# Kernel optimization log

Measured on AMD Instinct MI355X. Metric: run time of the kernel, lower is better.

The kernel has to match this reference:

```python
import jax, jax.numpy as jnp
import numpy as np

VOCAB = 267735
CUTOFFS = [0, 20000, 40000, 200000, 267735]
D_EMBED = 1024
D_PROJ = 1024
DIV_VAL = 4
EMB_SCALE = float(D_PROJ) ** 0.5


def setup_inputs() -> dict:
    key = jax.random.key(0)
    ks = jax.random.split(key, 9)
    input_ids = jax.random.randint(ks[0], (8, 2048), 0, VOCAB, dtype=jnp.int64)
    inp = {"input_ids": input_ids}
    for i in range(4):
        l, r = CUTOFFS[i], CUTOFFS[i + 1]
        d_i = D_EMBED // (DIV_VAL ** i)
        inp[f"emb{i}"] = jax.random.normal(ks[1 + 2 * i], (r - l, d_i), dtype=jnp.float32) * 0.02
        inp[f"proj{i}"] = jax.random.normal(ks[2 + 2 * i], (D_PROJ, d_i), dtype=jnp.float32) * 0.02
    return inp


def reference(input_ids, emb0, emb1, emb2, emb3, proj0, proj1, proj2, proj3):
    tables = [emb0, emb1, emb2, emb3]
    projs = [proj0, proj1, proj2, proj3]
    out = jnp.zeros(input_ids.shape + (D_PROJ,), dtype=jnp.float32)
    for i in range(4):
        l, r = CUTOFFS[i], CUTOFFS[i + 1]
        mask = (input_ids >= l) & (input_ids < r)                     # [B,S]
        idx = jnp.clip(input_ids - l, 0, r - l - 1)                   # [B,S]
        emb_i = tables[i][idx]                                        # [B,S,d_i]
        proj_i = jnp.einsum('bse,de->bsd', emb_i, projs[i])           # [B,S,D]
        out = out + jnp.where(mask[..., None], proj_i, 0.0)
    return out * EMB_SCALE
```

## Files before the change

### kernel.cpp

```cpp
#include <hip/hip_runtime.h>


constexpr int NTOK  = 16384;
constexpr int DPROJ = 1024;
constexpr float EMB_SCALE = 32.0f;

typedef __attribute__((ext_vector_type(8))) short short8;
typedef __attribute__((ext_vector_type(4))) float float4v;

__global__ __launch_bounds__(256) void partition_kernel(
    const int* __restrict__ ids, int* __restrict__ cnt, int* __restrict__ lists)
{
    int t = blockIdx.x * 256 + threadIdx.x;
    int id = ids[t];
    int c = (id >= 200000) ? 3 : (id >= 40000) ? 2 : (id >= 20000) ? 1 : 0;
    int lane = threadIdx.x & 63;
    unsigned long long lt = (1ull << lane) - 1ull;
    int pos = 0;
#pragma unroll
    for (int i = 0; i < 4; ++i) {
        unsigned long long m = __ballot(c == i);
        int b = 0;
        if (lane == 0 && m) b = atomicAdd(&cnt[i], (int)__popcll(m));
        b = __shfl(b, 0);
        if (c == i) pos = b + (int)__popcll(m & lt);
    }
    lists[c * NTOK + pos] = t;
}

__device__ __forceinline__ short f2bf(float f) {
    unsigned u = __builtin_bit_cast(unsigned, f);
    u += 0x7FFFu + ((u >> 16) & 1u);
    return (short)(u >> 16);
}

template<int D>
__device__ __forceinline__ void gemm_tile(
    const int* __restrict__ ids,
    const float* __restrict__ emb,
    const float* __restrict__ proj,
    const int* __restrict__ list,
    int count, int lo,
    float* __restrict__ out,
    short (*Asm)[40], short (*Bsm)[40], int* smTok, int* smRow)
{
    const int m0 = blockIdx.y * 64;
    if (m0 >= count) return;
    const int n0 = blockIdx.x * 128;
    const int tid  = threadIdx.x;
    const int lane = tid & 63;
    const int wv   = tid >> 6;
    const int col  = lane & 15;
    const int quad = lane >> 4;

    if (tid < 64) {
        int m = m0 + tid;
        int tok = (m < count) ? list[m] : -1;
        smTok[tid] = tok;
        smRow[tid] = (tok >= 0) ? (ids[tok] - lo) : 0;
    }
    __syncthreads();

    const int ar = tid >> 2, ac = (tid & 3) * 8;
    const int br = tid >> 1, bc = (tid & 1) * 16;
    const float* arow = emb  + (size_t)smRow[ar] * D + ac;
    const float* brow = proj + (size_t)(n0 + br) * D + bc;

    float4v acc[4][2] = {};

    constexpr int CHUNKS = (D + 31) / 32;
    for (int kc = 0; kc < CHUNKS; ++kc) {
        const int k0 = kc * 32;
        float4 a0 = {}, a1 = {}, b0 = {}, b1 = {}, b2 = {}, b3 = {};
        if (ac + 0  < D || D >= 32) {  }
        if (D >= 32 || ac + 0  < D) a0 = *(const float4*)(arow + k0);
        if (D >= 32 || ac + 4  < D) a1 = *(const float4*)(arow + k0 + 4);
        if (D >= 32 || bc + 0  < D) b0 = *(const float4*)(brow + k0);
        if (D >= 32 || bc + 4  < D) b1 = *(const float4*)(brow + k0 + 4);
        if (D >= 32 || bc + 8  < D) b2 = *(const float4*)(brow + k0 + 8);
        if (D >= 32 || bc + 12 < D) b3 = *(const float4*)(brow + k0 + 12);
        if (D == 16) {
            if (ac >= 16) { a0 = float4{}; a1 = float4{}; }
            if (bc >= 16) { b0 = float4{}; b1 = float4{}; b2 = float4{}; b3 = float4{}; }
        }
        __syncthreads();
        {
            short8 va = { f2bf(a0.x), f2bf(a0.y), f2bf(a0.z), f2bf(a0.w),
                          f2bf(a1.x), f2bf(a1.y), f2bf(a1.z), f2bf(a1.w) };
            *(short8*)&Asm[ar][ac] = va;
            short8 vb0 = { f2bf(b0.x), f2bf(b0.y), f2bf(b0.z), f2bf(b0.w),
                           f2bf(b1.x), f2bf(b1.y), f2bf(b1.z), f2bf(b1.w) };
            short8 vb1 = { f2bf(b2.x), f2bf(b2.y), f2bf(b2.z), f2bf(b2.w),
                           f2bf(b3.x), f2bf(b3.y), f2bf(b3.z), f2bf(b3.w) };
            *(short8*)&Bsm[br][bc]     = vb0;
            *(short8*)&Bsm[br][bc + 8] = vb1;
        }
        __syncthreads();

        short8 af[4], bf[2];
#pragma unroll
        for (int m = 0; m < 4; ++m)
            af[m] = *(const short8*)&Asm[m * 16 + col][quad * 8];
#pragma unroll
        for (int n = 0; n < 2; ++n)
            bf[n] = *(const short8*)&Bsm[wv * 32 + n * 16 + col][quad * 8];
#pragma unroll
        for (int m = 0; m < 4; ++m)
#pragma unroll
            for (int n = 0; n < 2; ++n)
                acc[m][n] = __builtin_amdgcn_mfma_f32_16x16x32_bf16(
                    af[m], bf[n], acc[m][n], 0, 0, 0);
    }

#pragma unroll
    for (int m = 0; m < 4; ++m) {
#pragma unroll
        for (int r = 0; r < 4; ++r) {
            int tok = smTok[m * 16 + quad * 4 + r];
            if (tok < 0) continue;
            float* op = out + (size_t)tok * DPROJ + n0 + wv * 32 + col;
            op[0]  = acc[m][0][r] * EMB_SCALE;
            op[16] = acc[m][1][r] * EMB_SCALE;
        }
    }
}

__global__ __launch_bounds__(256) void adaptive_emb_gemm(
    const int* __restrict__ ids,
    const float* __restrict__ e0, const float* __restrict__ p0,
    const float* __restrict__ e1, const float* __restrict__ p1,
    const float* __restrict__ e2, const float* __restrict__ p2,
    const float* __restrict__ e3, const float* __restrict__ p3,
    const int* __restrict__ cnt, const int* __restrict__ lists,
    float* __restrict__ out)
{
    __shared__ short Asm[64][40];
    __shared__ short Bsm[128][40];
    __shared__ int smTok[64];
    __shared__ int smRow[64];

    switch (blockIdx.z) {
    case 0: gemm_tile<1024>(ids, e0, p0, lists,          cnt[0], 0,      out, Asm, Bsm, smTok, smRow); break;
    case 1: gemm_tile<256> (ids, e1, p1, lists + NTOK,   cnt[1], 20000,  out, Asm, Bsm, smTok, smRow); break;
    case 2: gemm_tile<64>  (ids, e2, p2, lists + 2*NTOK, cnt[2], 40000,  out, Asm, Bsm, smTok, smRow); break;
    case 3: gemm_tile<16>  (ids, e3, p3, lists + 3*NTOK, cnt[3], 200000, out, Asm, Bsm, smTok, smRow); break;
    }
}

extern "C" void kernel_launch(void* const* d_in, const int* in_sizes, int n_in,
                              void* d_out, int out_size, void* d_ws, size_t ws_size,
                              hipStream_t stream) {
    const int*   ids = (const int*)d_in[0];
    const float* e0  = (const float*)d_in[1];
    const float* p0  = (const float*)d_in[2];
    const float* e1  = (const float*)d_in[3];
    const float* p1  = (const float*)d_in[4];
    const float* e2  = (const float*)d_in[5];
    const float* p2  = (const float*)d_in[6];
    const float* e3  = (const float*)d_in[7];
    const float* p3  = (const float*)d_in[8];
    float* out = (float*)d_out;

    int* cnt   = (int*)d_ws;
    int* lists = cnt + 4;

    hipMemsetAsync(cnt, 0, 4 * sizeof(int), stream);
    partition_kernel<<<dim3(NTOK / 256), 256, 0, stream>>>(ids, cnt, lists);

    dim3 grid(DPROJ / 128, NTOK / 64, 4);
    adaptive_emb_gemm<<<grid, 256, 0, stream>>>(
        ids, e0, p0, e1, p1, e2, p2, e3, p3, cnt, lists, out);
}
```

Before: 228.7 us.

## Pre-pack gathered embeddings and projections into bf16 MFMA fragment layout

New measurement: 238.3 us. +4.2%, slower.

```diff
diff --git a/kernel.cpp b/kernel.cpp
--- a/kernel.cpp
+++ b/kernel.cpp
@@ -7,6 +7,12 @@
 
 typedef __attribute__((ext_vector_type(8))) short short8;
 typedef __attribute__((ext_vector_type(4))) float float4v;
+
+__device__ __forceinline__ short f2bf(float f) {
+    unsigned u = __builtin_bit_cast(unsigned, f);
+    u += 0x7FFFu + ((u >> 16) & 1u);
+    return (short)(u >> 16);
+}
 
 __global__ __launch_bounds__(256) void partition_kernel(
     const int* __restrict__ ids, int* __restrict__ cnt, int* __restrict__ lists)
@@ -28,31 +34,163 @@
     lists[c * NTOK + pos] = t;
 }
 
-__device__ __forceinline__ short f2bf(float f) {
-    unsigned u = __builtin_bit_cast(unsigned, f);
-    u += 0x7FFFu + ((u >> 16) & 1u);
-    return (short)(u >> 16);
+
+__global__ __launch_bounds__(256) void pack_proj(
+    const float* __restrict__ p0, const float* __restrict__ p1,
+    const float* __restrict__ p2, const float* __restrict__ p3,
+    short* __restrict__ Bf)
+{
+    int t = blockIdx.x * 256 + threadIdx.x;
+    int c, local;
+    if      (t < 131072) { c = 0; local = t; }
+    else if (t < 163840) { c = 1; local = t - 131072; }
+    else if (t < 172032) { c = 2; local = t - 163840; }
+    else if (t < 176128) { c = 3; local = t - 172032; }
+    else return;
+    constexpr int Dc[4] = {1024, 256, 64, 16};
+    constexpr int Dp[4] = {1024, 256, 64, 32};
+    constexpr int SS[4] = {7, 5, 3, 2};
+    constexpr int BBase[4] = {0, 1048576, 1310720, 1376256};
+    const float* P[4] = {p0, p1, p2, p3};
+    int ss = SS[c];
+    int n = local >> ss;
+    int s = local & ((1 << ss) - 1);
+    int kc = s >> 2, q = s & 3;
+    int k0 = kc * 32 + q * 8;
+    int D = Dc[c], Dpad = Dp[c];
+    const float* src = P[c] + (size_t)n * D + k0;
+    short v[8];
+#pragma unroll
+    for (int j = 0; j < 8; ++j) v[j] = (k0 + j < D) ? f2bf(src[j]) : (short)0;
+    size_t dst = (size_t)BBase[c] + (size_t)(n >> 4) * (16 * Dpad)
+               + (size_t)kc * 512 + (q * 16 + (n & 15)) * 8;
+    *(short8*)(Bf + dst) = *(const short8*)v;
+}
+
+__global__ __launch_bounds__(256) void pack_A(
+    const int* __restrict__ ids, const int* __restrict__ cnt,
+    const int* __restrict__ lists,
+    const float* __restrict__ e0, const float* __restrict__ e1,
+    const float* __restrict__ e2, const float* __restrict__ e3,
+    short* __restrict__ Af)
+{
+    constexpr int Dc[4] = {1024, 256, 64, 16};
+    constexpr int Dp[4] = {1024, 256, 64, 32};
+    constexpr int SS[4] = {7, 5, 3, 2};
+    constexpr int lo[4] = {0, 20000, 40000, 200000};
+    const float* E[4] = {e0, e1, e2, e3};
+    int cv[4], P[4], W[5]; W[0] = 0;
+    size_t offA[4]; size_t a = 0;
+#pragma unroll
+    for (int c = 0; c < 4; ++c) {
+        cv[c] = cnt[c];
+        P[c]  = (cv[c] + 63) & ~63;
+        W[c + 1] = W[c] + (P[c] << SS[c]);
+        offA[c] = a; a += (size_t)P[c] * Dp[c];
+    }
+    int total = W[4];
+    for (int t = blockIdx.x * 256 + threadIdx.x; t < total; t += gridDim.x * 256) {
+        int c = (t >= W[1]) + (t >= W[2]) + (t >= W[3]);
+        int local = t - W[c];
+        int ss = SS[c];
+        int i = local >> ss;
+        int s = local & ((1 << ss) - 1);
+        int kc = s >> 2, q = s & 3;
+        int k0 = kc * 32 + q * 8;
+        int D = Dc[c], Dpad = Dp[c];
+        short v[8];
+        if (i < cv[c]) {
+            int tok = lists[c * NTOK + i];
+            int row = ids[tok] - lo[c];
+            const float* src = E[c] + (size_t)row * D + k0;
+#pragma unroll
+            for (int j = 0; j < 8; ++j) v[j] = (k0 + j < D) ? f2bf(src[j]) : (short)0;
+        } else {
+#pragma unroll
+            for (int j = 0; j < 8; ++j) v[j] = 0;
+        }
+        size_t dst = offA[c] + (size_t)(i >> 4) * (16 * Dpad)
+                   + (size_t)kc * 512 + (q * 16 + (i & 15)) * 8;
+        *(short8*)(Af + dst) = *(const short8*)v;
+    }
+}
+
+template<int DP>
+__device__ __forceinline__ void gemm_cluster(
+    const short* __restrict__ Af, const short* __restrict__ Bf,
+    const int* __restrict__ list, int count,
+    float* __restrict__ out, int* toks)
+{
+    const int x = blockIdx.x, y = blockIdx.y;
+    if (x * 256 >= count) return;
+    const int tid = threadIdx.x;
+    { int i = x * 256 + tid; toks[tid] = (i < count) ? list[i] : -1; }
+    __syncthreads();
+    const int w = tid >> 6, lane = tid & 63, col = lane & 15, quad = lane >> 4;
+    const int m0 = x * 256 + w * 64;
+    if (m0 >= count) return;
+    constexpr int CH = DP / 32;
+    const short* Ab = Af + (size_t)(m0 >> 4) * (16 * DP) + lane * 8;
+    const short* Bb = Bf + (size_t)(y * 4) * (16 * DP) + lane * 8;
+    float4v acc[4][4] = {};
+#pragma unroll 2
+    for (int kc = 0; kc < CH; ++kc) {
+        short8 af[4], bf[4];
+#pragma unroll
+        for (int m = 0; m < 4; ++m)
+            af[m] = *(const short8*)(Ab + (size_t)m * (16 * DP) + (size_t)kc * 512);
+#pragma unroll
+        for (int n = 0; n < 4; ++n)
+            bf[n] = *(const short8*)(Bb + (size_t)n * (16 * DP) + (size_t)kc * 512);
+#pragma unroll
+        for (int m = 0; m < 4; ++m)
+#pragma unroll
+            for (int n = 0; n < 4; ++n)
+                acc[m][n] = __builtin_amdgcn_mfma_f32_16x16x32_bf16(af[m], bf[n], acc[m][n], 0, 0, 0);
+    }
+#pragma unroll
+    for (int m = 0; m < 4; ++m)
+#pragma unroll
+        for (int r = 0; r < 4; ++r) {
+            int tok = toks[w * 64 + m * 16 + quad * 4 + r];
+            if (tok < 0) continue;
+            float* op = out + (size_t)tok * DPROJ + y * 64 + col;
+#pragma unroll
+            for (int n = 0; n < 4; ++n)
+                op[n * 16] = acc[m][n][r] * EMB_SCALE;
+        }
+}
+
+__global__ __launch_bounds__(256) void gemm_frag(
+    const int* __restrict__ cnt, const int* __restrict__ lists,
+    const short* __restrict__ Af, const short* __restrict__ Bf,
+    float* __restrict__ out)
+{
+    __shared__ int toks[256];
+    int P0 = (cnt[0] + 63) & ~63, P1 = (cnt[1] + 63) & ~63, P2 = (cnt[2] + 63) & ~63;
+    switch (blockIdx.z) {
+    case 0: gemm_cluster<1024>(Af, Bf, lists, cnt[0], out, toks); break;
+    case 1: gemm_cluster<256>(Af + (size_t)P0 * 1024, Bf + 1048576,
+                              lists + NTOK, cnt[1], out, toks); break;
+    case 2: gemm_cluster<64>(Af + (size_t)P0 * 1024 + (size_t)P1 * 256, Bf + 1310720,
+                             lists + 2 * NTOK, cnt[2], out, toks); break;
+    case 3: gemm_cluster<32>(Af + (size_t)P0 * 1024 + (size_t)P1 * 256 + (size_t)P2 * 64,
+                             Bf + 1376256, lists + 3 * NTOK, cnt[3], out, toks); break;
+    }
 }
 
 template<int D>
-__device__ __forceinline__ void gemm_tile(
-    const int* __restrict__ ids,
-    const float* __restrict__ emb,
-    const float* __restrict__ proj,
-    const int* __restrict__ list,
-    int count, int lo,
-    float* __restrict__ out,
+__device__ __forceinline__ void gemm_tile_fb(
+    const int* __restrict__ ids, const float* __restrict__ emb,
+    const float* __restrict__ proj, const int* __restrict__ list,
+    int count, int lo, float* __restrict__ out,
     short (*Asm)[40], short (*Bsm)[40], int* smTok, int* smRow)
 {
     const int m0 = blockIdx.y * 64;
     if (m0 >= count) return;
     const int n0 = blockIdx.x * 128;
-    const int tid  = threadIdx.x;
-    const int lane = tid & 63;
-    const int wv   = tid >> 6;
-    const int col  = lane & 15;
-    const int quad = lane >> 4;
-
+    const int tid = threadIdx.x, lane = tid & 63, wv = tid >> 6;
+    const int col = lane & 15, quad = lane >> 4;
     if (tid < 64) {
         int m = m0 + tid;
         int tok = (m < count) ? list[m] : -1;
@@ -60,60 +198,49 @@
         smRow[tid] = (tok >= 0) ? (ids[tok] - lo) : 0;
     }
     __syncthreads();
-
     const int ar = tid >> 2, ac = (tid & 3) * 8;
     const int br = tid >> 1, bc = (tid & 1) * 16;
     const float* arow = emb  + (size_t)smRow[ar] * D + ac;
     const float* brow = proj + (size_t)(n0 + br) * D + bc;
-
     float4v acc[4][2] = {};
-
     constexpr int CHUNKS = (D + 31) / 32;
     for (int kc = 0; kc < CHUNKS; ++kc) {
         const int k0 = kc * 32;
         float4 a0 = {}, a1 = {}, b0 = {}, b1 = {}, b2 = {}, b3 = {};
-        if (ac + 0  < D || D >= 32) {  }
-        if (D >= 32 || ac + 0  < D) a0 = *(const float4*)(arow + k0);
-        if (D >= 32 || ac + 4  < D) a1 = *(const float4*)(arow + k0 + 4);
-        if (D >= 32 || bc + 0  < D) b0 = *(const float4*)(brow + k0);
-        if (D >= 32 || bc + 4  < D) b1 = *(const float4*)(brow + k0 + 4);
-        if (D >= 32 || bc + 8  < D) b2 = *(const float4*)(brow + k0 + 8);
+        if (D >= 32 || ac < D)      a0 = *(const float4*)(arow + k0);
+        if (D >= 32 || ac + 4 < D)  a1 = *(const float4*)(arow + k0 + 4);
+        if (D >= 32 || bc < D)      b0 = *(const float4*)(brow + k0);
+        if (D >= 32 || bc + 4 < D)  b1 = *(const float4*)(brow + k0 + 4);
+        if (D >= 32 || bc + 8 < D)  b2 = *(const float4*)(brow + k0 + 8);
         if (D >= 32 || bc + 12 < D) b3 = *(const float4*)(brow + k0 + 12);
         if (D == 16) {
             if (ac >= 16) { a0 = float4{}; a1 = float4{}; }
             if (bc >= 16) { b0 = float4{}; b1 = float4{}; b2 = float4{}; b3 = float4{}; }
         }
         __syncthreads();
-        {
-            short8 va = { f2bf(a0.x), f2bf(a0.y), f2bf(a0.z), f2bf(a0.w),
-                          f2bf(a1.x), f2bf(a1.y), f2bf(a1.z), f2bf(a1.w) };
-            *(short8*)&Asm[ar][ac] = va;
-            short8 vb0 = { f2bf(b0.x), f2bf(b0.y), f2bf(b0.z), f2bf(b0.w),
-                           f2bf(b1.x), f2bf(b1.y), f2bf(b1.z), f2bf(b1.w) };
-            short8 vb1 = { f2bf(b2.x), f2bf(b2.y), f2bf(b2.z), f2bf(b2.w),
-                           f2bf(b3.x), f2bf(b3.y), f2bf(b3.z), f2bf(b3.w) };
-            *(short8*)&Bsm[br][bc]     = vb0;
-            *(short8*)&Bsm[br][bc + 8] = vb1;
-        }
+        short8 va = { f2bf(a0.x), f2bf(a0.y), f2bf(a0.z), f2bf(a0.w),
+                      f2bf(a1.x), f2bf(a1.y), f2bf(a1.z), f2bf(a1.w) };
+        *(short8*)&Asm[ar][ac] = va;
+        short8 vb0 = { f2bf(b0.x), f2bf(b0.y), f2bf(b0.z), f2bf(b0.w),
+                       f2bf(b1.x), f2bf(b1.y), f2bf(b1.z), f2bf(b1.w) };
+        short8 vb1 = { f2bf(b2.x), f2bf(b2.y), f2bf(b2.z), f2bf(b2.w),
+                       f2bf(b3.x), f2bf(b3.y), f2bf(b3.z), f2bf(b3.w) };
+        *(short8*)&Bsm[br][bc] = vb0;
+        *(short8*)&Bsm[br][bc + 8] = vb1;
         __syncthreads();
-
         short8 af[4], bf[2];
 #pragma unroll
+        for (int m = 0; m < 4; ++m) af[m] = *(const short8*)&Asm[m * 16 + col][quad * 8];
+#pragma unroll
+        for (int n = 0; n < 2; ++n) bf[n] = *(const short8*)&Bsm[wv * 32 + n * 16 + col][quad * 8];
+#pragma unroll
         for (int m = 0; m < 4; ++m)
-            af[m] = *(const short8*)&Asm[m * 16 + col][quad * 8];
-#pragma unroll
-        for (int n = 0; n < 2; ++n)
-            bf[n] = *(const short8*)&Bsm[wv * 32 + n * 16 + col][quad * 8];
-#pragma unroll
-        for (int m = 0; m < 4; ++m)
 #pragma unroll
             for (int n = 0; n < 2; ++n)
-                acc[m][n] = __builtin_amdgcn_mfma_f32_16x16x32_bf16(
-                    af[m], bf[n], acc[m][n], 0, 0, 0);
-    }
-
-#pragma unroll
-    for (int m = 0; m < 4; ++m) {
+                acc[m][n] = __builtin_amdgcn_mfma_f32_16x16x32_bf16(af[m], bf[n], acc[m][n], 0, 0, 0);
+    }
+#pragma unroll
+    for (int m = 0; m < 4; ++m)
 #pragma unroll
         for (int r = 0; r < 4; ++r) {
             int tok = smTok[m * 16 + quad * 4 + r];
@@ -122,10 +249,9 @@
             op[0]  = acc[m][0][r] * EMB_SCALE;
             op[16] = acc[m][1][r] * EMB_SCALE;
         }
-    }
-}
-
-__global__ __launch_bounds__(256) void adaptive_emb_gemm(
+}
+
+__global__ __launch_bounds__(256) void adaptive_emb_gemm_fb(
     const int* __restrict__ ids,
     const float* __restrict__ e0, const float* __restrict__ p0,
     const float* __restrict__ e1, const float* __restrict__ p1,
@@ -138,12 +264,11 @@
     __shared__ short Bsm[128][40];
     __shared__ int smTok[64];
     __shared__ int smRow[64];
-
     switch (blockIdx.z) {
-    case 0: gemm_tile<1024>(ids, e0, p0, lists,          cnt[0], 0,      out, Asm, Bsm, smTok, smRow); break;
-    case 1: gemm_tile<256> (ids, e1, p1, lists + NTOK,   cnt[1], 20000,  out, Asm, Bsm, smTok, smRow); break;
-    case 2: gemm_tile<64>  (ids, e2, p2, lists + 2*NTOK, cnt[2], 40000,  out, Asm, Bsm, smTok, smRow); break;
-    case 3: gemm_tile<16>  (ids, e3, p3, lists + 3*NTOK, cnt[3], 200000, out, Asm, Bsm, smTok, smRow); break;
+    case 0: gemm_tile_fb<1024>(ids, e0, p0, lists,          cnt[0], 0,      out, Asm, Bsm, smTok, smRow); break;
+    case 1: gemm_tile_fb<256> (ids, e1, p1, lists + NTOK,   cnt[1], 20000,  out, Asm, Bsm, smTok, smRow); break;
+    case 2: gemm_tile_fb<64>  (ids, e2, p2, lists + 2*NTOK, cnt[2], 40000,  out, Asm, Bsm, smTok, smRow); break;
+    case 3: gemm_tile_fb<16>  (ids, e3, p3, lists + 3*NTOK, cnt[3], 200000, out, Asm, Bsm, smTok, smRow); break;
     }
 }
 
@@ -164,10 +289,17 @@
     int* cnt   = (int*)d_ws;
     int* lists = cnt + 4;
 
-    hipMemsetAsync(cnt, 0, 4 * sizeof(int), stream);
+    hipMemsetAsync(cnt, 0, 16, stream);
     partition_kernel<<<dim3(NTOK / 256), 256, 0, stream>>>(ids, cnt, lists);
 
-    dim3 grid(DPROJ / 128, NTOK / 64, 4);
-    adaptive_emb_gemm<<<grid, 256, 0, stream>>>(
-        ids, e0, p0, e1, p1, e2, p2, e3, p3, cnt, lists, out);
-}
+    if (ws_size >= (size_t)40 * 1024 * 1024) {
+        short* Bf = (short*)((char*)d_ws + (512u << 10));
+        short* Af = (short*)((char*)d_ws + (4u << 20));
+        pack_proj<<<dim3(688), 256, 0, stream>>>(p0, p1, p2, p3, Bf);
+        pack_A<<<dim3(1024), 256, 0, stream>>>(ids, cnt, lists, e0, e1, e2, e3, Af);
+        gemm_frag<<<dim3(64, 16, 4), 256, 0, stream>>>(cnt, lists, Af, Bf, out);
+    } else {
+        adaptive_emb_gemm_fb<<<dim3(8, 256, 4), 256, 0, stream>>>(
+            ids, e0, p0, e1, p1, e2, p2, e3, p3, cnt, lists, out);
+    }
+}
```
